# Kernel tuning notes

Hardware: AMD Instinct MI355X
Metric: run time of the kernel (lower is better)

The kernel has to match this reference:

```python
import jax, jax.numpy as jnp
import numpy as np

DIM = 256
HEAD_DIM = 64
NH = DIM // HEAD_DIM
PS = 2  # fine patch size
EPS = 1e-5


def _conv(x, w, b, stride, pad):
    y = jax.lax.conv_general_dilated(x, w, (stride, stride), ((pad, pad), (pad, pad)),
                                     dimension_numbers=('NCHW', 'OIHW', 'NCHW'))
    return y + b[None, :, None, None]


def _bn(x, g, b, m, v):
    s = g * jax.lax.rsqrt(v + EPS)
    return x * s[None, :, None, None] + (b - m * s)[None, :, None, None]


def setup_inputs() -> dict:
    key = jax.random.key(0)
    ks = jax.random.split(key, 24)
    C = DIM
    d = {}
    d['x'] = jax.random.normal(ks[0], (8, C, 64, 64), jnp.float32)
    # Downsample conv (C->C, k=4, s=2, p=1), torch OIHW layout
    d['w_down'] = jax.random.normal(ks[1], (C, C, 4, 4), jnp.float32) * 0.02
    d['b_down'] = jax.random.normal(ks[2], (C,), jnp.float32) * 0.02
    # coarse to_qkv Linear(64 -> 192), stored as [in, out]
    d['w_qkv_c'] = jax.random.normal(ks[3], (HEAD_DIM, 3 * HEAD_DIM), jnp.float32) * 0.05
    d['b_qkv_c'] = jax.random.normal(ks[4], (3 * HEAD_DIM,), jnp.float32) * 0.02
    # Upsample ConvTranspose2d (torch [in, out, kH, kW] layout)
    d['w_up'] = jax.random.normal(ks[5], (C, C, 4, 4), jnp.float32) * 0.02
    d['b_up'] = jax.random.normal(ks[6], (C,), jnp.float32) * 0.02
    # fine to_qkv Linear(64 -> 192)
    d['w_qkv_f'] = jax.random.normal(ks[7], (HEAD_DIM, 3 * HEAD_DIM), jnp.float32) * 0.05
    d['b_qkv_f'] = jax.random.normal(ks[8], (3 * HEAD_DIM,), jnp.float32) * 0.02
    # DWConv: depthwise 3x3 (groups=C) -> BN -> relu6 -> pointwise 1x1 -> BN -> relu6
    d['w_dw'] = jax.random.normal(ks[9], (C, 1, 3, 3), jnp.float32) * 0.1
    d['bn_dw_g'] = jax.random.uniform(ks[10], (C,), jnp.float32) * 0.5 + 0.75
    d['bn_dw_b'] = jax.random.normal(ks[11], (C,), jnp.float32) * 0.1
    d['bn_dw_m'] = jax.random.normal(ks[12], (C,), jnp.float32) * 0.1
    d['bn_dw_v'] = jax.random.uniform(ks[13], (C,), jnp.float32) + 0.5
    d['w_pw'] = jax.random.normal(ks[14], (C, C, 1, 1), jnp.float32) * 0.05
    d['bn_pw_g'] = jax.random.uniform(ks[15], (C,), jnp.float32) * 0.5 + 0.75
    d['bn_pw_b'] = jax.random.normal(ks[16], (C,), jnp.float32) * 0.1
    d['bn_pw_m'] = jax.random.normal(ks[17], (C,), jnp.float32) * 0.1
    d['bn_pw_v'] = jax.random.uniform(ks[18], (C,), jnp.float32) + 0.5
    return d


def reference(x, w_down, b_down, w_qkv_c, b_qkv_c, w_up, b_up, w_qkv_f, b_qkv_f,
              w_dw, bn_dw_g, bn_dw_b, bn_dw_m, bn_dw_v,
              w_pw, bn_pw_g, bn_pw_b, bn_pw_m, bn_pw_v):
    B, C, H, W = x.shape
    nh, hd = C // HEAD_DIM, HEAD_DIM
    scale = hd ** -0.5

    # ---- CoarseSelfAttention ----
    xd = _conv(x, w_down, b_down, 2, 1)           # [B,C,h,w]
    h, w = xd.shape[2], xd.shape[3]
    P = h * w
    tok = xd.reshape(B, nh, hd, P).transpose(0, 1, 3, 2)   # [B,nh,P,hd]
    q, k, v = jnp.split(tok @ w_qkv_c + b_qkv_c, 3, axis=-1)
    attn = jax.nn.softmax(jnp.einsum('bhqd,bhkd->bhqk', q, k) * scale, axis=-1)
    coarse_score = attn.sum(axis=-2)               # [B,nh,P]
    kf = max(1, P // 4)
    top_k = jax.lax.top_k(coarse_score, kf)[1]     # [B,nh,kf]
    out = jnp.einsum('bhqk,bhkd->bhqd', attn, v)
    out = out.transpose(0, 1, 3, 2).reshape(B, C, h, w)
    # ConvTranspose2d(k=4,s=2,p=1) as lhs-dilated conv with flipped/transposed kernel
    wt = jnp.flip(w_up, (2, 3)).transpose(1, 0, 2, 3)
    coarse = jax.lax.conv_general_dilated(out, wt, (1, 1), ((2, 2), (2, 2)),
                                          lhs_dilation=(2, 2),
                                          dimension_numbers=('NCHW', 'OIHW', 'NCHW'))
    coarse = coarse + b_up[None, :, None, None]
    # F.interpolate to (H,W) is identity here: upsample exactly restores HxW

    # ---- TopkSelfAttention ----
    ph, pw = H // PS, W // PS                      # ph*pw == P
    xh = coarse.reshape(B, nh, hd, ph, PS, pw, PS)
    patches = xh.transpose(0, 1, 2, 3, 5, 4, 6).reshape(B, nh, hd, ph * pw, PS, PS)
    idx = jnp.broadcast_to(top_k[:, :, None, :, None, None], (B, nh, hd, kf, PS, PS))
    sel = jnp.take_along_axis(patches, idx, axis=3)        # [B,nh,hd,kf,PS,PS]
    tokf = sel.reshape(B, nh, hd, kf, PS * PS).transpose(0, 1, 3, 4, 2)
    tokf = tokf.reshape(B, nh, kf * PS * PS, hd)
    qf, kk, vf = jnp.split(tokf @ w_qkv_f + b_qkv_f, 3, axis=-1)
    attnf = jax.nn.softmax(jnp.einsum('bhqd,bhkd->bhqk', qf, kk) * scale, axis=-1)
    outf = jnp.einsum('bhqk,bhkd->bhqd', attnf, vf)
    outf = outf.reshape(B, nh, kf, PS * PS, hd).transpose(0, 1, 2, 4, 3)
    outf = outf.reshape(B, nh, kf, hd, PS, PS)     # [B,nh,kf,hd,PS,PS]
    # scatter selected patches back into zeros (topk indices are unique per b,h)
    res = jnp.zeros((B, nh, ph * pw, hd, PS, PS), x.dtype)
    bi = jnp.arange(B)[:, None, None]
    hi = jnp.arange(nh)[None, :, None]
    res = res.at[bi, hi, top_k].set(outf)
    res = res.transpose(0, 1, 3, 2, 4, 5).reshape(B, nh, hd, ph, pw, PS, PS)
    region = res.transpose(0, 1, 2, 3, 5, 4, 6).reshape(B, C, H, W)

    y = coarse + region

    # ---- DWConv feed-forward ----
    yd = jax.lax.conv_general_dilated(y, w_dw, (1, 1), ((1, 1), (1, 1)),
                                      feature_group_count=C,
                                      dimension_numbers=('NCHW', 'OIHW', 'NCHW'))
    yd = jnp.clip(_bn(yd, bn_dw_g, bn_dw_b, bn_dw_m, bn_dw_v), 0.0, 6.0)
    yp = jax.lax.conv_general_dilated(yd, w_pw, (1, 1), ((0, 0), (0, 0)),
                                      dimension_numbers=('NCHW', 'OIHW', 'NCHW'))
    yp = jnp.clip(_bn(yp, bn_pw_g, bn_pw_b, bn_pw_m, bn_pw_v), 0.0, 6.0)
    return yp
```

## Files before the change

kernel.cpp:

```cpp
#include <hip/hip_runtime.h>
#include <cstdint>
#include <cstddef>


#define EPS_ 1e-5f

typedef short bf16x8_t __attribute__((ext_vector_type(8)));
typedef float f32x4_t __attribute__((ext_vector_type(4)));
#define MFMA16(a, b, c) __builtin_amdgcn_mfma_f32_16x16x32_bf16(a, b, c, 0, 0, 0)

__device__ __forceinline__ void cvt1(float f, unsigned short& h, unsigned short& l) {
  unsigned u = __float_as_uint(f);
  unsigned r = u + 0x7FFFu + ((u >> 16) & 1u);
  h = (unsigned short)(r >> 16);
  float lo = f - __uint_as_float(r & 0xFFFF0000u);
  l = (unsigned short)(__float_as_uint(lo) >> 16);
}
__device__ __forceinline__ unsigned cvtpack(float f) {
  unsigned short h, l;
  cvt1(f, h, l);
  return (unsigned)h | ((unsigned)l << 16);
}
__device__ __forceinline__ void cvt2(float f0, float f1, unsigned& hpack, unsigned& lpack) {
  unsigned u0 = __float_as_uint(f0), u1 = __float_as_uint(f1);
  unsigned r0 = u0 + 0x7FFFu + ((u0 >> 16) & 1u);
  unsigned r1 = u1 + 0x7FFFu + ((u1 >> 16) & 1u);
  hpack = (r0 >> 16) | (r1 & 0xFFFF0000u);
  float l0 = f0 - __uint_as_float(r0 & 0xFFFF0000u);
  float l1 = f1 - __uint_as_float(r1 & 0xFFFF0000u);
  lpack = (__float_as_uint(l0) >> 16) | (__float_as_uint(l1) & 0xFFFF0000u);
}
__device__ __forceinline__ unsigned pk_h(unsigned a, unsigned b) {
  return (a & 0xFFFFu) | (b << 16);
}
__device__ __forceinline__ unsigned pk_l(unsigned a, unsigned b) {
  return (a >> 16) | (b & 0xFFFF0000u);
}

__global__ __launch_bounds__(256) void k_pad_x(
    const float* __restrict__ x, unsigned* __restrict__ xphl) {
  const int plane = blockIdx.x;
  const float* src = x + (size_t)plane * 4096;
  unsigned* dst = xphl + (size_t)plane * 4488;
  for (int e = threadIdx.x; e < 4356; e += 256) {
    int r = e / 66, cc = e - r * 66;
    float v = 0.f;
    if (r >= 1 && r <= 64 && cc >= 1 && cc <= 64) v = src[(r - 1) * 64 + (cc - 1)];
    dst[r * 68 + cc] = cvtpack(v);
  }
}

__global__ __launch_bounds__(256) void k_cvt_wdown(
    const float* __restrict__ w, unsigned short* __restrict__ wh,
    unsigned short* __restrict__ wl) {
  int e = blockIdx.x * 256 + threadIdx.x;
  cvt1(w[e], wh[e], wl[e]);
}

__global__ __launch_bounds__(256) void k_cvt_wqkv(
    const float* __restrict__ wq, unsigned short* __restrict__ wh,
    unsigned short* __restrict__ wl) {
  int e = blockIdx.x * 256 + threadIdx.x;
  int col = e >> 6, d = e & 63;
  float f = wq[d * 192 + col];
  if (col < 64) f *= 0.125f;
  cvt1(f, wh[e], wl[e]);
}

__global__ __launch_bounds__(256) void k_cvt_wup(
    const float* __restrict__ w_up, unsigned short* __restrict__ wth,
    unsigned short* __restrict__ wtl) {
  int e = blockIdx.x * 256 + threadIdx.x;
  int kp = e & 1023, oc = (e >> 10) & 255, c = e >> 18;
  int tap = kp >> 8, ic = kp & 255;
  int tk = tap >> 1, txi = tap & 1;
  int ry = c >> 1, rx = c & 1;
  int ky = (1 - ry) + 2 * tk, kx = (1 - rx) + 2 * txi;
  cvt1(w_up[((size_t)(ic * 256 + oc) * 4 + ky) * 4 + kx], wth[e], wtl[e]);
}

__global__ __launch_bounds__(256) void k_cvt_wpw(
    const float* __restrict__ w, unsigned short* __restrict__ wh,
    unsigned short* __restrict__ wl) {
  int e = blockIdx.x * 256 + threadIdx.x;
  cvt1(w[e], wh[e], wl[e]);
}

__device__ __forceinline__ void mfma_chunk(
    const unsigned short (*Ah)[72], const unsigned short (*Al)[72],
    const unsigned short (*Bh)[72], const unsigned short (*Bl)[72],
    f32x4_t (&acc)[4], int wm, int lane) {
  const int l16 = lane & 15, quad = lane >> 4;
#pragma unroll
  for (int ks = 0; ks < 2; ++ks) {
    int ko = ks * 32 + quad * 8;
    bf16x8_t ah = *(const bf16x8_t*)&Ah[wm + l16][ko];
    bf16x8_t al = *(const bf16x8_t*)&Al[wm + l16][ko];
#pragma unroll
    for (int nt = 0; nt < 4; ++nt) {
      bf16x8_t bh = *(const bf16x8_t*)&Bh[nt * 16 + l16][ko];
      bf16x8_t bl = *(const bf16x8_t*)&Bl[nt * 16 + l16][ko];
      acc[nt] = MFMA16(ah, bh, acc[nt]);
      acc[nt] = MFMA16(ah, bl, acc[nt]);
      acc[nt] = MFMA16(al, bh, acc[nt]);
    }
  }
}

__device__ __forceinline__ void mfma_tile2x2(
    const unsigned short (*Ah)[72], const unsigned short (*Al)[72],
    const unsigned short (*Bh)[72], const unsigned short (*Bl)[72],
    f32x4_t (&acc)[2][2], int wm, int wn, int lane) {
  const int l16 = lane & 15, quad = lane >> 4;
#pragma unroll
  for (int ks = 0; ks < 2; ++ks) {
    int ko = ks * 32 + quad * 8;
    bf16x8_t ah[2], al[2];
#pragma unroll
    for (int mt = 0; mt < 2; ++mt) {
      ah[mt] = *(const bf16x8_t*)&Ah[wm + mt * 16 + l16][ko];
      al[mt] = *(const bf16x8_t*)&Al[wm + mt * 16 + l16][ko];
    }
#pragma unroll
    for (int nt = 0; nt < 2; ++nt) {
      bf16x8_t bh = *(const bf16x8_t*)&Bh[wn + nt * 16 + l16][ko];
      bf16x8_t bl = *(const bf16x8_t*)&Bl[wn + nt * 16 + l16][ko];
#pragma unroll
      for (int mt = 0; mt < 2; ++mt) {
        acc[mt][nt] = MFMA16(ah[mt], bh, acc[mt][nt]);
        acc[mt][nt] = MFMA16(ah[mt], bl, acc[mt][nt]);
        acc[mt][nt] = MFMA16(al[mt], bh, acc[mt][nt]);
      }
    }
  }
}

__device__ __forceinline__ void mfma_tile2x4(
    const unsigned short (*Ah)[72], const unsigned short (*Al)[72],
    const unsigned short (*Bh)[72], const unsigned short (*Bl)[72],
    f32x4_t (&acc)[2][4], int wm, int wn, int lane) {
  const int l16 = lane & 15, quad = lane >> 4;
#pragma unroll
  for (int ks = 0; ks < 2; ++ks) {
    int ko = ks * 32 + quad * 8;
    bf16x8_t ah[2], al[2];
#pragma unroll
    for (int mt = 0; mt < 2; ++mt) {
      ah[mt] = *(const bf16x8_t*)&Ah[wm + mt * 16 + l16][ko];
      al[mt] = *(const bf16x8_t*)&Al[wm + mt * 16 + l16][ko];
    }
#pragma unroll
    for (int nt = 0; nt < 4; ++nt) {
      bf16x8_t bh = *(const bf16x8_t*)&Bh[wn + nt * 16 + l16][ko];
      bf16x8_t bl = *(const bf16x8_t*)&Bl[wn + nt * 16 + l16][ko];
#pragma unroll
      for (int mt = 0; mt < 2; ++mt) {
        acc[mt][nt] = MFMA16(ah[mt], bh, acc[mt][nt]);
        acc[mt][nt] = MFMA16(ah[mt], bl, acc[mt][nt]);
        acc[mt][nt] = MFMA16(al[mt], bh, acc[mt][nt]);
      }
    }
  }
}

__global__ __launch_bounds__(256) void k_conv_down_mfma(
    const unsigned* __restrict__ xphl, const unsigned short* __restrict__ wdh,
    const unsigned short* __restrict__ wdl, const float* __restrict__ bias,
    unsigned* __restrict__ xdhl) {
  __shared__ unsigned short Ah[64][72], Al[64][72], Bh[64][72], Bl[64][72];
  const int t = threadIdx.x;
  const int pix0 = blockIdx.x * 64, oc0 = blockIdx.y * 64;
  const int bimg = pix0 >> 10, pos = pix0 & 1023;
  const int pl = t & 63, icg = t >> 6;
  const int rem = (pix0 + pl) & 1023;
  const int oy = rem >> 5, ox = rem & 31;
  const unsigned* xb = xphl + ((size_t)bimg * 256 + icg) * 4488 + (oy * 2) * 68 + ox * 2;
  const int wave = t >> 6, lane = t & 63, l16 = lane & 15, quad = lane >> 4;
  const int wm = (wave & 1) * 32, wn = (wave >> 1) * 32;
  const int ar = t >> 2, ac = (t & 3) * 16;
  const unsigned short* wra = wdh + (size_t)(oc0 + ar) * 4096 + ac;
  const unsigned short* wrl = wdl + (size_t)(oc0 + ar) * 4096 + ac;
  f32x4_t acc[2][2] = {};
  for (int kb = 0; kb < 4096; kb += 64) {
    bf16x8_t a0 = *(const bf16x8_t*)(wra + kb);
    bf16x8_t a1 = *(const bf16x8_t*)(wra + kb + 8);
    bf16x8_t a2 = *(const bf16x8_t*)(wrl + kb);
    bf16x8_t a3 = *(const bf16x8_t*)(wrl + kb + 8);
    unsigned u[16];
#pragma unroll
    for (int r = 0; r < 4; ++r) {
      uint2 u01 = *(const uint2*)(xb + r * 68);
      uint2 u23 = *(const uint2*)(xb + r * 68 + 2);
      u[4 * r + 0] = u01.x; u[4 * r + 1] = u01.y;
      u[4 * r + 2] = u23.x; u[4 * r + 3] = u23.y;
    }
    unsigned hp[8], lp[8];
#pragma unroll
    for (int j = 0; j < 8; ++j) {
      hp[j] = pk_h(u[2 * j], u[2 * j + 1]);
      lp[j] = pk_l(u[2 * j], u[2 * j + 1]);
    }
    __syncthreads();
    *(bf16x8_t*)&Ah[ar][ac] = a0;
    *(bf16x8_t*)&Ah[ar][ac + 8] = a1;
    *(bf16x8_t*)&Al[ar][ac] = a2;
    *(bf16x8_t*)&Al[ar][ac + 8] = a3;
    *(uint4*)&Bh[pl][icg * 16] = make_uint4(hp[0], hp[1], hp[2], hp[3]);
    *(uint4*)&Bh[pl][icg * 16 + 8] = make_uint4(hp[4], hp[5], hp[6], hp[7]);
    *(uint4*)&Bl[pl][icg * 16] = make_uint4(lp[0], lp[1], lp[2], lp[3]);
    *(uint4*)&Bl[pl][icg * 16 + 8] = make_uint4(lp[4], lp[5], lp[6], lp[7]);
    __syncthreads();
    mfma_tile2x2(Ah, Al, Bh, Bl, acc, wm, wn, lane);
    xb += 4 * 4488;
  }
#pragma unroll
  for (int mt = 0; mt < 2; ++mt)
#pragma unroll
    for (int r = 0; r < 4; ++r) {
      int oc = oc0 + wm + mt * 16 + quad * 4 + r;
      float bv = bias[oc];
#pragma unroll
      for (int nt = 0; nt < 2; ++nt)
        xdhl[((size_t)(bimg * 256 + oc)) * 1024 + pos + wn + nt * 16 + l16] =
            cvtpack(acc[mt][nt][r] + bv);
    }
}

template <int MODE>
__global__ __launch_bounds__(256) void k_qkv_mfma(
    const unsigned* __restrict__ srcp, const float* __restrict__ srcf,
    const unsigned short* __restrict__ wh, const unsigned short* __restrict__ wl,
    const float* __restrict__ bq, const int* __restrict__ topk,
    unsigned short* __restrict__ qh, unsigned short* __restrict__ ql,
    unsigned short* __restrict__ kh, unsigned short* __restrict__ kl,
    unsigned short* __restrict__ vth, unsigned short* __restrict__ vtl) {
  __shared__ unsigned short Ah[64][72], Al[64][72];
  const int t = threadIdx.x;
  const int tok0 = blockIdx.x * 64;
  const int pair = blockIdx.y;
  const int b = pair >> 2, h = pair & 3;
  const int tokl = t & 63, dg = t >> 6;
  unsigned hp[8], lp[8];
  if (MODE == 0) {
    const unsigned* base = srcp + ((size_t)(b * 256 + h * 64 + dg * 16)) * 1024 + tok0 + tokl;
    unsigned u[16];
#pragma unroll
    for (int j = 0; j < 16; ++j) u[j] = base[(size_t)j * 1024];
#pragma unroll
    for (int j = 0; j < 8; ++j) {
      hp[j] = pk_h(u[2 * j], u[2 * j + 1]);
      lp[j] = pk_l(u[2 * j], u[2 * j + 1]);
    }
  } else {
    int tok = tok0 + tokl;
    int pp = topk[pair * 256 + (tok >> 2)];
    int py = (tok >> 1) & 1, px = tok & 1;
    int ry = (pp >> 5) * 2 + py, rx = (pp & 31) * 2 + px;
    const float* base = srcf + ((size_t)(b * 256 + h * 64 + dg * 16)) * 4096 + ry * 64 + rx;
    float fv[16];
#pragma unroll
    for (int j = 0; j < 16; ++j) fv[j] = base[(size_t)j * 4096];
#pragma unroll
    for (int j = 0; j < 8; ++j) cvt2(fv[2 * j], fv[2 * j + 1], hp[j], lp[j]);
  }
  *(uint4*)&Ah[tokl][dg * 16] = make_uint4(hp[0], hp[1], hp[2], hp[3]);
  *(uint4*)&Ah[tokl][dg * 16 + 8] = make_uint4(hp[4], hp[5], hp[6], hp[7]);
  *(uint4*)&Al[tokl][dg * 16] = make_uint4(lp[0], lp[1], lp[2], lp[3]);
  *(uint4*)&Al[tokl][dg * 16 + 8] = make_uint4(lp[4], lp[5], lp[6], lp[7]);
  __syncthreads();
  const int wave = t >> 6, lane = t & 63, l16 = lane & 15, quad = lane >> 4;
  f32x4_t acc[4][3] = {};
#pragma unroll
  for (int ks = 0; ks < 2; ++ks) {
    int ko = ks * 32 + quad * 8;
    bf16x8_t bh0[3], bl0[3];
#pragma unroll
    for (int nt = 0; nt < 3; ++nt) {
      int col = wave * 48 + nt * 16 + l16;
      bh0[nt] = *(const bf16x8_t*)(wh + col * 64 + ko);
      bl0[nt] = *(const bf16x8_t*)(wl + col * 64 + ko);
    }
#pragma unroll
    for (int mt = 0; mt < 4; ++mt) {
      bf16x8_t ah = *(const bf16x8_t*)&Ah[mt * 16 + l16][ko];
      bf16x8_t al = *(const bf16x8_t*)&Al[mt * 16 + l16][ko];
#pragma unroll
      for (int nt = 0; nt < 3; ++nt) {
        acc[mt][nt] = MFMA16(ah, bh0[nt], acc[mt][nt]);
        acc[mt][nt] = MFMA16(ah, bl0[nt], acc[mt][nt]);
        acc[mt][nt] = MFMA16(al, bh0[nt], acc[mt][nt]);
      }
    }
  }
#pragma unroll
  for (int nt = 0; nt < 3; ++nt) {
    int col = wave * 48 + nt * 16 + l16;
    float bqv = bq[col];
    if (col < 64) bqv *= 0.125f;
#pragma unroll
    for (int mt = 0; mt < 4; ++mt) {
#pragma unroll
      for (int r = 0; r < 4; ++r) {
        int tok = tok0 + mt * 16 + quad * 4 + r;
        float val = acc[mt][nt][r] + bqv;
        unsigned short hh, ll;
        cvt1(val, hh, ll);
        if (col < 64) {
          size_t o = ((size_t)pair * 1024 + tok) * 64 + col;
          qh[o] = hh; ql[o] = ll;
        } else if (col < 128) {
          size_t o = ((size_t)pair * 1024 + tok) * 64 + (col - 64);
          kh[o] = hh; kl[o] = ll;
        } else {
          size_t o = ((size_t)pair * 64 + (col - 128)) * 1024 + tok;
          vth[o] = hh; vtl[o] = ll;
        }
      }
    }
  }
}

template <int COARSE>
__global__ __launch_bounds__(256) void k_attn(
    const unsigned short* __restrict__ qh, const unsigned short* __restrict__ ql,
    const unsigned short* __restrict__ kh, const unsigned short* __restrict__ kl,
    const unsigned short* __restrict__ vth, const unsigned short* __restrict__ vtl,
    float* __restrict__ score, unsigned* __restrict__ outc,
    float* __restrict__ outf) {
  __shared__ __align__(16) unsigned short Qb[2][64][72];
  __shared__ __align__(16) unsigned short Kb[2][64][72];
  __shared__ __align__(16) unsigned short Pb[2][64][72];
  __shared__ float mlW[4][2][64];
  __shared__ float mC[64], lC[64];
  __shared__ float colsum[1024];
  const int t = threadIdx.x;
  const int q0 = blockIdx.x * 64;
  const int pair = blockIdx.y;
  const int wave = t >> 6, lane = t & 63;
  const int l16 = lane & 15, quad = lane >> 4;
  const int wm = wave * 16;
  const int sr = t >> 3, skc = (t & 7) * 8;

  const size_t qbase = ((size_t)pair * 1024 + q0) * 64;
#pragma unroll
  for (int i = 0; i < 2; ++i) {
    int r = sr + i * 32;
    *(bf16x8_t*)&Qb[0][r][skc] = *(const bf16x8_t*)(qh + qbase + (size_t)r * 64 + skc);
    *(bf16x8_t*)&Qb[1][r][skc] = *(const bf16x8_t*)(ql + qbase + (size_t)r * 64 + skc);
  }
  if (COARSE) {
#pragma unroll
    for (int i = 0; i < 4; ++i) colsum[t + i * 256] = 0.f;
  }

  const size_t kmbase = (size_t)pair * 1024 * 64;
  const size_t vbase = (size_t)pair * 64 * 1024;

  float mrun[4] = {-1e30f, -1e30f, -1e30f, -1e30f};
  float lrun[4] = {0.f, 0.f, 0.f, 0.f};
  for (int kb = 0; kb < 1024; kb += 64) {
    __syncthreads();
#pragma unroll
    for (int i = 0; i < 2; ++i) {
      int r = sr + i * 32;
      *(bf16x8_t*)&Kb[0][r][skc] = *(const bf16x8_t*)(kh + kmbase + (size_t)(kb + r) * 64 + skc);
      *(bf16x8_t*)&Kb[1][r][skc] = *(const bf16x8_t*)(kl + kmbase + (size_t)(kb + r) * 64 + skc);
    }
    __syncthreads();
    f32x4_t acc[4] = {};
    mfma_chunk(Kb[0], Kb[1], Qb[0], Qb[1], acc, wm, lane);
#pragma unroll
    for (int nt = 0; nt < 4; ++nt) {
      float m0 = fmaxf(fmaxf(acc[nt][0], acc[nt][1]), fmaxf(acc[nt][2], acc[nt][3]));
      m0 = fmaxf(m0, __shfl_xor(m0, 16));
      m0 = fmaxf(m0, __shfl_xor(m0, 32));
      float mn = fmaxf(mrun[nt], m0);
      float s0 = __expf(acc[nt][0] - mn) + __expf(acc[nt][1] - mn) +
                 __expf(acc[nt][2] - mn) + __expf(acc[nt][3] - mn);
      s0 += __shfl_xor(s0, 16);
      s0 += __shfl_xor(s0, 32);
      lrun[nt] = lrun[nt] * __expf(mrun[nt] - mn) + s0;
      mrun[nt] = mn;
    }
  }
  __syncthreads();
  if (quad == 0) {
#pragma unroll
    for (int nt = 0; nt < 4; ++nt) {
      mlW[wave][0][nt * 16 + l16] = mrun[nt];
      mlW[wave][1][nt * 16 + l16] = lrun[nt];
    }
  }
  __syncthreads();
  if (t < 64) {
    float m0 = mlW[0][0][t], m1 = mlW[1][0][t], m2 = mlW[2][0][t], m3 = mlW[3][0][t];
    float mm = fmaxf(fmaxf(m0, m1), fmaxf(m2, m3));
    float ll = mlW[0][1][t] * __expf(m0 - mm) + mlW[1][1][t] * __expf(m1 - mm) +
               mlW[2][1][t] * __expf(m2 - mm) + mlW[3][1][t] * __expf(m3 - mm);
    mC[t] = mm;
    lC[t] = 1.0f / ll;
  }
  __syncthreads();
  float mq[4], il[4];
#pragma unroll
  for (int nt = 0; nt < 4; ++nt) {
    mq[nt] = mC[nt * 16 + l16];
    il[nt] = lC[nt * 16 + l16];
  }

  f32x4_t accO[4] = {};
  for (int kb = 0; kb < 1024; kb += 64) {
    __syncthreads();
#pragma unroll
    for (int i = 0; i < 2; ++i) {
      int r = sr + i * 32;
      *(bf16x8_t*)&Kb[0][r][skc] = *(const bf16x8_t*)(kh + kmbase + (size_t)(kb + r) * 64 + skc);
      *(bf16x8_t*)&Kb[1][r][skc] = *(const bf16x8_t*)(kl + kmbase + (size_t)(kb + r) * 64 + skc);
    }
    __syncthreads();
    f32x4_t acc[4] = {};
    mfma_chunk(Kb[0], Kb[1], Qb[0], Qb[1], acc, wm, lane);
    float P[4][4];
#pragma unroll
    for (int nt = 0; nt < 4; ++nt)
#pragma unroll
      for (int r = 0; r < 4; ++r) P[nt][r] = __expf(acc[nt][r] - mq[nt]) * il[nt];
    if (COARSE) {
#pragma unroll
      for (int r = 0; r < 4; ++r) {
        float cs = P[0][r] + P[1][r] + P[2][r] + P[3][r];
        cs += __shfl_xor(cs, 1);
        cs += __shfl_xor(cs, 2);
        cs += __shfl_xor(cs, 4);
        cs += __shfl_xor(cs, 8);
        if (l16 == 0) colsum[kb + wm + quad * 4 + r] += cs;
      }
    }
    __syncthreads();
#pragma unroll
    for (int nt = 0; nt < 4; ++nt) {
      unsigned h01, l01, h23, l23;
      cvt2(P[nt][0], P[nt][1], h01, l01);
      cvt2(P[nt][2], P[nt][3], h23, l23);
      *(uint2*)&Pb[0][nt * 16 + l16][wm + quad * 4] = make_uint2(h01, h23);
      *(uint2*)&Pb[1][nt * 16 + l16][wm + quad * 4] = make_uint2(l01, l23);
    }
#pragma unroll
    for (int i = 0; i < 2; ++i) {
      int r = sr + i * 32;
      *(bf16x8_t*)&Kb[0][r][skc] = *(const bf16x8_t*)(vth + vbase + (size_t)r * 1024 + kb + skc);
      *(bf16x8_t*)&Kb[1][r][skc] = *(const bf16x8_t*)(vtl + vbase + (size_t)r * 1024 + kb + skc);
    }
    __syncthreads();
    mfma_chunk(Pb[0], Pb[1], Kb[0], Kb[1], accO, wm, lane);
  }
  __syncthreads();

  if (COARSE) {
#pragma unroll
    for (int i = 0; i < 4; ++i)
      atomicAdd(&score[pair * 1024 + t + i * 256], colsum[t + i * 256]);
    float (*Tr)[68] = reinterpret_cast<float(*)[68]>(&Pb[0][0][0]);
#pragma unroll
    for (int nt = 0; nt < 4; ++nt)
#pragma unroll
      for (int r = 0; r < 4; ++r)
        Tr[nt * 16 + l16][wm + quad * 4 + r] = accO[nt][r];
    __syncthreads();
    const int b = pair >> 2, h = pair & 3;
#pragma unroll
    for (int i = 0; i < 16; ++i) {
      int e = t + i * 256;
      int d = e >> 6, ql_ = e & 63;
      int pix = q0 + ql_;
      int iy = (pix >> 5) + 1, ix = (pix & 31) + 1;
      outc[((size_t)(b * 256 + h * 64 + d)) * 1156 + iy * 34 + ix] = cvtpack(Tr[d][ql_]);
    }
  } else {
#pragma unroll
    for (int nt = 0; nt < 4; ++nt)
#pragma unroll
      for (int r = 0; r < 4; ++r) {
        int qm = q0 + wm + quad * 4 + r;
        outf[((size_t)pair * 1024 + qm) * 64 + nt * 16 + l16] = accO[nt][r];
      }
  }
}

__global__ __launch_bounds__(256) void k_topk(
    const float* __restrict__ score, int* __restrict__ idx) {
  __shared__ unsigned long long key[1024];
  const int pair = blockIdx.x;
  const int t = threadIdx.x;
#pragma unroll
  for (int j = 0; j < 4; ++j) {
    int i = t + j * 256;
    unsigned u = __float_as_uint(score[pair * 1024 + i]);
    u = u ^ ((u & 0x80000000u) ? 0xFFFFFFFFu : 0x80000000u);
    u = ~u;
    key[i] = ((unsigned long long)u << 32) | (unsigned)i;
  }
  __syncthreads();
  for (int k = 2; k <= 1024; k <<= 1) {
    for (int j = k >> 1; j > 0; j >>= 1) {
      for (int w = 0; w < 4; ++w) {
        int i = t + w * 256;
        int l = i ^ j;
        if (l > i) {
          bool up = ((i & k) == 0);
          unsigned long long a = key[i], b = key[l];
          if ((a > b) == up) { key[i] = b; key[l] = a; }
        }
      }
      __syncthreads();
    }
  }
  idx[pair * 256 + t] = (int)(key[t] & 0xFFFFFFFFu);
}

__global__ __launch_bounds__(256) void k_convT_mfma(
    const unsigned* __restrict__ inp, const unsigned short* __restrict__ wth,
    const unsigned short* __restrict__ wtl, const float* __restrict__ bias,
    float* __restrict__ out) {
  __shared__ unsigned short Ah[64][72], Al[64][72];
  __shared__ unsigned short Bh[128][72], Bl[128][72];
  const int t = threadIdx.x;
  const int pix0 = blockIdx.x * 128;
  const int oc0 = blockIdx.y * 64;
  const int cls = blockIdx.z;
  const int ry = cls >> 1, rx = cls & 1;
  const int b = pix0 >> 10;
  const int wave = t >> 6, lane = t & 63;
  const int l16 = lane & 15, quad = lane >> 4;
  const int wm = (wave & 1) * 32, wn = (wave >> 1) * 64;
  const int pl = t & 127, icg = t >> 7;
  const int remg = (pix0 + pl) & 1023;
  const int tyy = remg >> 5, txx = remg & 31;
  const int ar = t >> 2, ac = (t & 3) * 16;
  const size_t wbase = ((size_t)cls * 256 + oc0 + ar) * 1024 + ac;
  f32x4_t acc[2][4] = {};
  for (int kb = 0; kb < 1024; kb += 64) {
    const int tap = kb >> 8, ic0 = kb & 255;
    const int tk = tap >> 1, txi = tap & 1;
    const int iy = tyy + ry + 1 - tk, ix = txx + rx + 1 - txi;
    const unsigned* p = inp + (size_t)(b * 256 + ic0 + icg * 32) * 1156 + iy * 34 + ix;
    unsigned u[32];
#pragma unroll
    for (int j = 0; j < 32; ++j) u[j] = p[(size_t)j * 1156];
    unsigned hp[16], lpk[16];
#pragma unroll
    for (int j = 0; j < 16; ++j) {
      hp[j] = pk_h(u[2 * j], u[2 * j + 1]);
      lpk[j] = pk_l(u[2 * j], u[2 * j + 1]);
    }
    bf16x8_t a0 = *(const bf16x8_t*)(wth + wbase + kb);
    bf16x8_t a1 = *(const bf16x8_t*)(wth + wbase + kb + 8);
    bf16x8_t a2 = *(const bf16x8_t*)(wtl + wbase + kb);
    bf16x8_t a3 = *(const bf16x8_t*)(wtl + wbase + kb + 8);
    __syncthreads();
    *(bf16x8_t*)&Ah[ar][ac] = a0;
    *(bf16x8_t*)&Ah[ar][ac + 8] = a1;
    *(bf16x8_t*)&Al[ar][ac] = a2;
    *(bf16x8_t*)&Al[ar][ac + 8] = a3;
    {
      int kc = icg * 32;
      *(uint4*)&Bh[pl][kc] = make_uint4(hp[0], hp[1], hp[2], hp[3]);
      *(uint4*)&Bh[pl][kc + 8] = make_uint4(hp[4], hp[5], hp[6], hp[7]);
      *(uint4*)&Bh[pl][kc + 16] = make_uint4(hp[8], hp[9], hp[10], hp[11]);
      *(uint4*)&Bh[pl][kc + 24] = make_uint4(hp[12], hp[13], hp[14], hp[15]);
      *(uint4*)&Bl[pl][kc] = make_uint4(lpk[0], lpk[1], lpk[2], lpk[3]);
      *(uint4*)&Bl[pl][kc + 8] = make_uint4(lpk[4], lpk[5], lpk[6], lpk[7]);
      *(uint4*)&Bl[pl][kc + 16] = make_uint4(lpk[8], lpk[9], lpk[10], lpk[11]);
      *(uint4*)&Bl[pl][kc + 24] = make_uint4(lpk[12], lpk[13], lpk[14], lpk[15]);
    }
    __syncthreads();
    mfma_tile2x4(Ah, Al, Bh, Bl, acc, wm, wn, lane);
  }
#pragma unroll
  for (int mt = 0; mt < 2; ++mt)
#pragma unroll
    for (int r = 0; r < 4; ++r) {
      int oc = oc0 + wm + mt * 16 + quad * 4 + r;
      float bvs = bias[oc];
#pragma unroll
      for (int nt = 0; nt < 4; ++nt) {
        int pix = pix0 + wn + nt * 16 + l16;
        int rem2 = pix & 1023;
        int y = (rem2 >> 5) * 2 + ry, xx = (rem2 & 31) * 2 + rx;
        out[((size_t)(b * 256 + oc) * 64 + y) * 64 + xx] = acc[mt][nt][r] + bvs;
      }
    }
}

__global__ __launch_bounds__(256) void k_scatter(
    const float* __restrict__ outf, const int* __restrict__ idx,
    float* __restrict__ y) {
  int g = blockIdx.x * 256 + threadIdx.x;
  int pair = g >> 16;
  int rem = g & 65535;
  int tok = rem >> 6, d = rem & 63;
  int b = pair >> 2, h = pair & 3;
  int pp = idx[pair * 256 + (tok >> 2)];
  int py = (tok >> 1) & 1, px = tok & 1;
  int ry = (pp >> 5) * 2 + py, rx = (pp & 31) * 2 + px;
  y[((size_t)(b * 256 + h * 64 + d) * 64 + ry) * 64 + rx] += outf[g];
}

__global__ __launch_bounds__(256) void k_dwconv(
    const float* __restrict__ y, const float* __restrict__ wdw,
    const float* __restrict__ g, const float* __restrict__ bb,
    const float* __restrict__ m, const float* __restrict__ vv,
    unsigned* __restrict__ ydhl) {
  int gi = blockIdx.x * 256 + threadIdx.x;
  int x = gi & 63, yy = (gi >> 6) & 63, ch = (gi >> 12) & 255, b = gi >> 20;
  const float* plane = y + (size_t)(b * 256 + ch) * 4096;
  const float* wc = wdw + ch * 9;
  float s = 0.f;
#pragma unroll
  for (int ky = 0; ky < 3; ++ky) {
    int iy = yy + ky - 1;
    if (iy < 0 || iy >= 64) continue;
#pragma unroll
    for (int kx = 0; kx < 3; ++kx) {
      int ix = x + kx - 1;
      if (ix < 0 || ix >= 64) continue;
      s = fmaf(plane[iy * 64 + ix], wc[ky * 3 + kx], s);
    }
  }
  float sc = g[ch] * rsqrtf(vv[ch] + EPS_);
  float val = s * sc + (bb[ch] - m[ch] * sc);
  ydhl[gi] = cvtpack(fminf(fmaxf(val, 0.f), 6.f));
}

__global__ __launch_bounds__(256) void k_pw_mfma(
    const unsigned* __restrict__ ydhl, const unsigned short* __restrict__ wh,
    const unsigned short* __restrict__ wl, const float* __restrict__ g,
    const float* __restrict__ bb, const float* __restrict__ m,
    const float* __restrict__ vv, float* __restrict__ out) {
  __shared__ unsigned short Ah[64][72], Al[64][72];
  __shared__ unsigned short Bh[128][72], Bl[128][72];
  const int t = threadIdx.x;
  const int pix0 = blockIdx.x * 128;
  const int oc0 = blockIdx.y * 64;
  const int b = pix0 >> 12, pos0 = pix0 & 4095;
  const int wave = t >> 6, lane = t & 63;
  const int l16 = lane & 15, quad = lane >> 4;
  const int wm = (wave & 1) * 32, wn = (wave >> 1) * 64;
  const int pl = t & 127, icg = t >> 7;
  const int ar = t >> 2, ac = (t & 3) * 16;
  f32x4_t acc[2][4] = {};
  for (int kb = 0; kb < 256; kb += 64) {
    const unsigned* p = ydhl + (size_t)(b * 256 + kb + icg * 32) * 4096 + pos0 + pl;
    unsigned u[32];
#pragma unroll
    for (int j = 0; j < 32; ++j) u[j] = p[(size_t)j * 4096];
    unsigned hp[16], lpk[16];
#pragma unroll
    for (int j = 0; j < 16; ++j) {
      hp[j] = pk_h(u[2 * j], u[2 * j + 1]);
      lpk[j] = pk_l(u[2 * j], u[2 * j + 1]);
    }
    bf16x8_t a0 = *(const bf16x8_t*)(wh + (size_t)(oc0 + ar) * 256 + kb + ac);
    bf16x8_t a1 = *(const bf16x8_t*)(wh + (size_t)(oc0 + ar) * 256 + kb + ac + 8);
    bf16x8_t a2 = *(const bf16x8_t*)(wl + (size_t)(oc0 + ar) * 256 + kb + ac);
    bf16x8_t a3 = *(const bf16x8_t*)(wl + (size_t)(oc0 + ar) * 256 + kb + ac + 8);
    __syncthreads();
    *(bf16x8_t*)&Ah[ar][ac] = a0;
    *(bf16x8_t*)&Ah[ar][ac + 8] = a1;
    *(bf16x8_t*)&Al[ar][ac] = a2;
    *(bf16x8_t*)&Al[ar][ac + 8] = a3;
    {
      int kc = icg * 32;
      *(uint4*)&Bh[pl][kc] = make_uint4(hp[0], hp[1], hp[2], hp[3]);
      *(uint4*)&Bh[pl][kc + 8] = make_uint4(hp[4], hp[5], hp[6], hp[7]);
      *(uint4*)&Bh[pl][kc + 16] = make_uint4(hp[8], hp[9], hp[10], hp[11]);
      *(uint4*)&Bh[pl][kc + 24] = make_uint4(hp[12], hp[13], hp[14], hp[15]);
      *(uint4*)&Bl[pl][kc] = make_uint4(lpk[0], lpk[1], lpk[2], lpk[3]);
      *(uint4*)&Bl[pl][kc + 8] = make_uint4(lpk[4], lpk[5], lpk[6], lpk[7]);
      *(uint4*)&Bl[pl][kc + 16] = make_uint4(lpk[8], lpk[9], lpk[10], lpk[11]);
      *(uint4*)&Bl[pl][kc + 24] = make_uint4(lpk[12], lpk[13], lpk[14], lpk[15]);
    }
    __syncthreads();
    mfma_tile2x4(Ah, Al, Bh, Bl, acc, wm, wn, lane);
  }
#pragma unroll
  for (int mt = 0; mt < 2; ++mt)
#pragma unroll
    for (int r = 0; r < 4; ++r) {
      int oc = oc0 + wm + mt * 16 + quad * 4 + r;
      float sc = g[oc] * rsqrtf(vv[oc] + EPS_);
      float off = bb[oc] - m[oc] * sc;
#pragma unroll
      for (int nt = 0; nt < 4; ++nt) {
        int pix = pos0 + wn + nt * 16 + l16;
        float val = fminf(fmaxf(acc[mt][nt][r] * sc + off, 0.f), 6.f);
        out[(size_t)(b * 256 + oc) * 4096 + pix] = val;
      }
    }
}

extern "C" void kernel_launch(void* const* d_in, const int* in_sizes, int n_in,
                              void* d_out, int out_size, void* d_ws, size_t ws_size,
                              hipStream_t stream) {
  (void)in_sizes; (void)n_in; (void)out_size; (void)ws_size;
  const float* x       = (const float*)d_in[0];
  const float* w_down  = (const float*)d_in[1];
  const float* b_down  = (const float*)d_in[2];
  const float* w_qkv_c = (const float*)d_in[3];
  const float* b_qkv_c = (const float*)d_in[4];
  const float* w_up    = (const float*)d_in[5];
  const float* b_up    = (const float*)d_in[6];
  const float* w_qkv_f = (const float*)d_in[7];
  const float* b_qkv_f = (const float*)d_in[8];
  const float* w_dw    = (const float*)d_in[9];
  const float* bn_dw_g = (const float*)d_in[10];
  const float* bn_dw_b = (const float*)d_in[11];
  const float* bn_dw_m = (const float*)d_in[12];
  const float* bn_dw_v = (const float*)d_in[13];
  const float* w_pw    = (const float*)d_in[14];
  const float* bn_pw_g = (const float*)d_in[15];
  const float* bn_pw_b = (const float*)d_in[16];
  const float* bn_pw_m = (const float*)d_in[17];
  const float* bn_pw_v = (const float*)d_in[18];

  float* ws = (float*)d_ws;
  unsigned*       xphl   = (unsigned*)ws;
  unsigned*       ydhl   = (unsigned*)ws;
  unsigned short* qh     = (unsigned short*)(ws + 33554432);
  unsigned short* ql     = (unsigned short*)(ws + 34603008);
  unsigned short* kh     = (unsigned short*)(ws + 35651584);
  unsigned short* kl     = (unsigned short*)(ws + 36700160);
  unsigned short* vth    = (unsigned short*)(ws + 37748736);
  unsigned short* vtl    = (unsigned short*)(ws + 38797312);
  unsigned*       xdhl   = (unsigned*)(ws + 39845888);
  unsigned*       outcphl= (unsigned*)(ws + 41943040);
  float*          coarse = ws + 44310528;
  float*          outf   = ws + 52699136;
  float*          score  = ws + 54796288;
  unsigned short* wdh    = (unsigned short*)(ws + 54829056);
  unsigned short* wdl    = (unsigned short*)(ws + 55353344);
  unsigned short* wt_hi  = (unsigned short*)(ws + 55877632);
  unsigned short* wt_lo  = (unsigned short*)(ws + 56401920);
  unsigned short* wpw_hi = (unsigned short*)(ws + 56926208);
  unsigned short* wpw_lo = (unsigned short*)(ws + 56958976);
  unsigned short* wqh_c  = (unsigned short*)(ws + 56991744);
  unsigned short* wql_c  = (unsigned short*)(ws + 56997888);
  unsigned short* wqh_f  = (unsigned short*)(ws + 57004032);
  unsigned short* wql_f  = (unsigned short*)(ws + 57010176);
  int*            idx    = (int*)(ws + 57016320);

  hipMemsetAsync(score, 0, 32768 * sizeof(float), stream);
  hipMemsetAsync(outcphl, 0, (size_t)2367488 * sizeof(unsigned), stream);
  k_pad_x<<<2048, 256, 0, stream>>>(x, xphl);
  k_cvt_wdown<<<4096, 256, 0, stream>>>(w_down, wdh, wdl);
  k_cvt_wqkv<<<48, 256, 0, stream>>>(w_qkv_c, wqh_c, wql_c);
  k_cvt_wqkv<<<48, 256, 0, stream>>>(w_qkv_f, wqh_f, wql_f);
  k_cvt_wup<<<4096, 256, 0, stream>>>(w_up, wt_hi, wt_lo);
  k_cvt_wpw<<<256, 256, 0, stream>>>(w_pw, wpw_hi, wpw_lo);

  k_conv_down_mfma<<<dim3(128, 4), 256, 0, stream>>>(xphl, wdh, wdl, b_down, xdhl);
  k_qkv_mfma<0><<<dim3(16, 32), 256, 0, stream>>>(xdhl, nullptr, wqh_c, wql_c, b_qkv_c,
                                                  nullptr, qh, ql, kh, kl, vth, vtl);
  k_attn<1><<<dim3(16, 32), 256, 0, stream>>>(qh, ql, kh, kl, vth, vtl, score,
                                              outcphl, nullptr);
  k_topk<<<32, 256, 0, stream>>>(score, idx);
  k_convT_mfma<<<dim3(64, 4, 4), 256, 0, stream>>>(outcphl, wt_hi, wt_lo, b_up, coarse);

  k_qkv_mfma<1><<<dim3(16, 32), 256, 0, stream>>>(nullptr, coarse, wqh_f, wql_f, b_qkv_f,
                                                  idx, qh, ql, kh, kl, vth, vtl);
  k_attn<0><<<dim3(16, 32), 256, 0, stream>>>(qh, ql, kh, kl, vth, vtl, nullptr,
                                              nullptr, outf);
  k_scatter<<<8192, 256, 0, stream>>>(outf, idx, coarse);
  k_dwconv<<<32768, 256, 0, stream>>>(coarse, w_dw, bn_dw_g, bn_dw_b, bn_dw_m, bn_dw_v, ydhl);
  k_pw_mfma<<<dim3(256, 4), 256, 0, stream>>>(ydhl, wpw_hi, wpw_lo, bn_pw_g, bn_pw_b,
                                              bn_pw_m, bn_pw_v, (float*)d_out);
}
```

Measured before the change: 617.0 us.

## Use single-pass online softmax for fine attention and co-load V with K

```diff
diff --git a/kernel.cpp b/kernel.cpp
--- a/kernel.cpp
+++ b/kernel.cpp
@@ -320,15 +320,14 @@
   }
 }
 
-template <int COARSE>
-__global__ __launch_bounds__(256) void k_attn(
+__global__ __launch_bounds__(256) void k_attn_coarse(
     const unsigned short* __restrict__ qh, const unsigned short* __restrict__ ql,
     const unsigned short* __restrict__ kh, const unsigned short* __restrict__ kl,
     const unsigned short* __restrict__ vth, const unsigned short* __restrict__ vtl,
-    float* __restrict__ score, unsigned* __restrict__ outc,
-    float* __restrict__ outf) {
+    float* __restrict__ score, unsigned* __restrict__ outc) {
   __shared__ __align__(16) unsigned short Qb[2][64][72];
   __shared__ __align__(16) unsigned short Kb[2][64][72];
+  __shared__ __align__(16) unsigned short Vb[2][64][72];
   __shared__ __align__(16) unsigned short Pb[2][64][72];
   __shared__ float mlW[4][2][64];
   __shared__ float mC[64], lC[64];
@@ -348,10 +347,8 @@
     *(bf16x8_t*)&Qb[0][r][skc] = *(const bf16x8_t*)(qh + qbase + (size_t)r * 64 + skc);
     *(bf16x8_t*)&Qb[1][r][skc] = *(const bf16x8_t*)(ql + qbase + (size_t)r * 64 + skc);
   }
-  if (COARSE) {
-#pragma unroll
-    for (int i = 0; i < 4; ++i) colsum[t + i * 256] = 0.f;
-  }
+#pragma unroll
+  for (int i = 0; i < 4; ++i) colsum[t + i * 256] = 0.f;
 
   const size_t kmbase = (size_t)pair * 1024 * 64;
   const size_t vbase = (size_t)pair * 64 * 1024;
@@ -416,6 +413,8 @@
       int r = sr + i * 32;
       *(bf16x8_t*)&Kb[0][r][skc] = *(const bf16x8_t*)(kh + kmbase + (size_t)(kb + r) * 64 + skc);
       *(bf16x8_t*)&Kb[1][r][skc] = *(const bf16x8_t*)(kl + kmbase + (size_t)(kb + r) * 64 + skc);
+      *(bf16x8_t*)&Vb[0][r][skc] = *(const bf16x8_t*)(vth + vbase + (size_t)r * 1024 + kb + skc);
+      *(bf16x8_t*)&Vb[1][r][skc] = *(const bf16x8_t*)(vtl + vbase + (size_t)r * 1024 + kb + skc);
     }
     __syncthreads();
     f32x4_t acc[4] = {};
@@ -425,18 +424,15 @@
     for (int nt = 0; nt < 4; ++nt)
 #pragma unroll
       for (int r = 0; r < 4; ++r) P[nt][r] = __expf(acc[nt][r] - mq[nt]) * il[nt];
-    if (COARSE) {
-#pragma unroll
-      for (int r = 0; r < 4; ++r) {
-        float cs = P[0][r] + P[1][r] + P[2][r] + P[3][r];
-        cs += __shfl_xor(cs, 1);
-        cs += __shfl_xor(cs, 2);
-        cs += __shfl_xor(cs, 4);
-        cs += __shfl_xor(cs, 8);
-        if (l16 == 0) colsum[kb + wm + quad * 4 + r] += cs;
-      }
-    }
-    __syncthreads();
+#pragma unroll
+    for (int r = 0; r < 4; ++r) {
+      float cs = P[0][r] + P[1][r] + P[2][r] + P[3][r];
+      cs += __shfl_xor(cs, 1);
+      cs += __shfl_xor(cs, 2);
+      cs += __shfl_xor(cs, 4);
+      cs += __shfl_xor(cs, 8);
+      if (l16 == 0) colsum[kb + wm + quad * 4 + r] += cs;
+    }
 #pragma unroll
     for (int nt = 0; nt < 4; ++nt) {
       unsigned h01, l01, h23, l23;
@@ -445,45 +441,127 @@
       *(uint2*)&Pb[0][nt * 16 + l16][wm + quad * 4] = make_uint2(h01, h23);
       *(uint2*)&Pb[1][nt * 16 + l16][wm + quad * 4] = make_uint2(l01, l23);
     }
+    __syncthreads();
+    mfma_chunk(Pb[0], Pb[1], Vb[0], Vb[1], accO, wm, lane);
+  }
+  __syncthreads();
+
+#pragma unroll
+  for (int i = 0; i < 4; ++i)
+    atomicAdd(&score[pair * 1024 + t + i * 256], colsum[t + i * 256]);
+  float (*Tr)[68] = reinterpret_cast<float(*)[68]>(&Pb[0][0][0]);
+#pragma unroll
+  for (int nt = 0; nt < 4; ++nt)
+#pragma unroll
+    for (int r = 0; r < 4; ++r)
+      Tr[nt * 16 + l16][wm + quad * 4 + r] = accO[nt][r];
+  __syncthreads();
+  const int b = pair >> 2, h = pair & 3;
+#pragma unroll
+  for (int i = 0; i < 16; ++i) {
+    int e = t + i * 256;
+    int d = e >> 6, ql_ = e & 63;
+    int pix = q0 + ql_;
+    int iy = (pix >> 5) + 1, ix = (pix & 31) + 1;
+    outc[((size_t)(b * 256 + h * 64 + d)) * 1156 + iy * 34 + ix] = cvtpack(Tr[d][ql_]);
+  }
+}
+
+__global__ __launch_bounds__(256) void k_attn_fine(
+    const unsigned short* __restrict__ qh, const unsigned short* __restrict__ ql,
+    const unsigned short* __restrict__ kh, const unsigned short* __restrict__ kl,
+    const unsigned short* __restrict__ vth, const unsigned short* __restrict__ vtl,
+    float* __restrict__ outf) {
+  __shared__ __align__(16) unsigned short Qb[2][64][72];
+  __shared__ __align__(16) unsigned short Kb[2][64][72];
+  __shared__ __align__(16) unsigned short Vb[2][64][72];
+  __shared__ __align__(16) unsigned short Pb[2][64][72];
+  __shared__ float m_run[64], l_run[64], alphaS[64];
+  __shared__ float mWc[4][64], sWc[4][64];
+  const int t = threadIdx.x;
+  const int q0 = blockIdx.x * 64;
+  const int pair = blockIdx.y;
+  const int wave = t >> 6, lane = t & 63;
+  const int l16 = lane & 15, quad = lane >> 4;
+  const int wm = wave * 16;
+  const int sr = t >> 3, skc = (t & 7) * 8;
+
+  const size_t qbase = ((size_t)pair * 1024 + q0) * 64;
+#pragma unroll
+  for (int i = 0; i < 2; ++i) {
+    int r = sr + i * 32;
+    *(bf16x8_t*)&Qb[0][r][skc] = *(const bf16x8_t*)(qh + qbase + (size_t)r * 64 + skc);
+    *(bf16x8_t*)&Qb[1][r][skc] = *(const bf16x8_t*)(ql + qbase + (size_t)r * 64 + skc);
+  }
+  if (t < 64) { m_run[t] = -1e30f; l_run[t] = 0.f; }
+
+  const size_t kmbase = (size_t)pair * 1024 * 64;
+  const size_t vbase = (size_t)pair * 64 * 1024;
+
+  f32x4_t accO[4] = {};
+  for (int kb = 0; kb < 1024; kb += 64) {
+    __syncthreads();
 #pragma unroll
     for (int i = 0; i < 2; ++i) {
       int r = sr + i * 32;
-      *(bf16x8_t*)&Kb[0][r][skc] = *(const bf16x8_t*)(vth + vbase + (size_t)r * 1024 + kb + skc);
-      *(bf16x8_t*)&Kb[1][r][skc] = *(const bf16x8_t*)(vtl + vbase + (size_t)r * 1024 + kb + skc);
-    }
-    __syncthreads();
-    mfma_chunk(Pb[0], Pb[1], Kb[0], Kb[1], accO, wm, lane);
+      *(bf16x8_t*)&Kb[0][r][skc] = *(const bf16x8_t*)(kh + kmbase + (size_t)(kb + r) * 64 + skc);
+      *(bf16x8_t*)&Kb[1][r][skc] = *(const bf16x8_t*)(kl + kmbase + (size_t)(kb + r) * 64 + skc);
+      *(bf16x8_t*)&Vb[0][r][skc] = *(const bf16x8_t*)(vth + vbase + (size_t)r * 1024 + kb + skc);
+      *(bf16x8_t*)&Vb[1][r][skc] = *(const bf16x8_t*)(vtl + vbase + (size_t)r * 1024 + kb + skc);
+    }
+    __syncthreads();
+    f32x4_t acc[4] = {};
+    mfma_chunk(Kb[0], Kb[1], Qb[0], Qb[1], acc, wm, lane);
+#pragma unroll
+    for (int nt = 0; nt < 4; ++nt) {
+      float m0 = fmaxf(fmaxf(acc[nt][0], acc[nt][1]), fmaxf(acc[nt][2], acc[nt][3]));
+      m0 = fmaxf(m0, __shfl_xor(m0, 16));
+      m0 = fmaxf(m0, __shfl_xor(m0, 32));
+      if (quad == 0) mWc[wave][nt * 16 + l16] = m0;
+    }
+    __syncthreads();
+    if (t < 64) {
+      float mn = fmaxf(fmaxf(fmaxf(mWc[0][t], mWc[1][t]), fmaxf(mWc[2][t], mWc[3][t])),
+                       m_run[t]);
+      alphaS[t] = __expf(m_run[t] - mn);
+      m_run[t] = mn;
+    }
+    __syncthreads();
+    float P[4][4];
+#pragma unroll
+    for (int nt = 0; nt < 4; ++nt) {
+      float mn = m_run[nt * 16 + l16];
+#pragma unroll
+      for (int r = 0; r < 4; ++r) P[nt][r] = __expf(acc[nt][r] - mn);
+      float s0 = P[nt][0] + P[nt][1] + P[nt][2] + P[nt][3];
+      s0 += __shfl_xor(s0, 16);
+      s0 += __shfl_xor(s0, 32);
+      if (quad == 0) sWc[wave][nt * 16 + l16] = s0;
+      unsigned h01, l01, h23, l23;
+      cvt2(P[nt][0], P[nt][1], h01, l01);
+      cvt2(P[nt][2], P[nt][3], h23, l23);
+      *(uint2*)&Pb[0][nt * 16 + l16][wm + quad * 4] = make_uint2(h01, h23);
+      *(uint2*)&Pb[1][nt * 16 + l16][wm + quad * 4] = make_uint2(l01, l23);
+    }
+#pragma unroll
+    for (int r = 0; r < 4; ++r) {
+      float a = alphaS[wm + quad * 4 + r];
+#pragma unroll
+      for (int nt = 0; nt < 4; ++nt) accO[nt][r] *= a;
+    }
+    __syncthreads();
+    if (t < 64)
+      l_run[t] = l_run[t] * alphaS[t] + (sWc[0][t] + sWc[1][t] + sWc[2][t] + sWc[3][t]);
+    mfma_chunk(Pb[0], Pb[1], Vb[0], Vb[1], accO, wm, lane);
   }
   __syncthreads();
-
-  if (COARSE) {
-#pragma unroll
-    for (int i = 0; i < 4; ++i)
-      atomicAdd(&score[pair * 1024 + t + i * 256], colsum[t + i * 256]);
-    float (*Tr)[68] = reinterpret_cast<float(*)[68]>(&Pb[0][0][0]);
+#pragma unroll
+  for (int r = 0; r < 4; ++r) {
+    float invl = 1.0f / l_run[wm + quad * 4 + r];
+    int qm = q0 + wm + quad * 4 + r;
 #pragma unroll
     for (int nt = 0; nt < 4; ++nt)
-#pragma unroll
-      for (int r = 0; r < 4; ++r)
-        Tr[nt * 16 + l16][wm + quad * 4 + r] = accO[nt][r];
-    __syncthreads();
-    const int b = pair >> 2, h = pair & 3;
-#pragma unroll
-    for (int i = 0; i < 16; ++i) {
-      int e = t + i * 256;
-      int d = e >> 6, ql_ = e & 63;
-      int pix = q0 + ql_;
-      int iy = (pix >> 5) + 1, ix = (pix & 31) + 1;
-      outc[((size_t)(b * 256 + h * 64 + d)) * 1156 + iy * 34 + ix] = cvtpack(Tr[d][ql_]);
-    }
-  } else {
-#pragma unroll
-    for (int nt = 0; nt < 4; ++nt)
-#pragma unroll
-      for (int r = 0; r < 4; ++r) {
-        int qm = q0 + wm + quad * 4 + r;
-        outf[((size_t)pair * 1024 + qm) * 64 + nt * 16 + l16] = accO[nt][r];
-      }
+      outf[((size_t)pair * 1024 + qm) * 64 + nt * 16 + l16] = accO[nt][r] * invl;
   }
 }
 
@@ -761,15 +839,13 @@
   k_conv_down_mfma<<<dim3(128, 4), 256, 0, stream>>>(xphl, wdh, wdl, b_down, xdhl);
   k_qkv_mfma<0><<<dim3(16, 32), 256, 0, stream>>>(xdhl, nullptr, wqh_c, wql_c, b_qkv_c,
                                                   nullptr, qh, ql, kh, kl, vth, vtl);
-  k_attn<1><<<dim3(16, 32), 256, 0, stream>>>(qh, ql, kh, kl, vth, vtl, score,
-                                              outcphl, nullptr);
+  k_attn_coarse<<<dim3(16, 32), 256, 0, stream>>>(qh, ql, kh, kl, vth, vtl, score, outcphl);
   k_topk<<<32, 256, 0, stream>>>(score, idx);
   k_convT_mfma<<<dim3(64, 4, 4), 256, 0, stream>>>(outcphl, wt_hi, wt_lo, b_up, coarse);
 
   k_qkv_mfma<1><<<dim3(16, 32), 256, 0, stream>>>(nullptr, coarse, wqh_f, wql_f, b_qkv_f,
                                                   idx, qh, ql, kh, kl, vth, vtl);
-  k_attn<0><<<dim3(16, 32), 256, 0, stream>>>(qh, ql, kh, kl, vth, vtl, nullptr,
-                                              nullptr, outf);
+  k_attn_fine<<<dim3(16, 32), 256, 0, stream>>>(qh, ql, kh, kl, vth, vtl, outf);
   k_scatter<<<8192, 256, 0, stream>>>(outf, idx, coarse);
   k_dwconv<<<32768, 256, 0, stream>>>(coarse, w_dw, bn_dw_g, bn_dw_b, bn_dw_m, bn_dw_v, ydhl);
   k_pw_mfma<<<dim3(256, 4), 256, 0, stream>>>(ydhl, wpw_hi, wpw_lo, bn_pw_g, bn_pw_b,
```

Result: no change. 611.7 us (-0.9%).
